# Optimization experiments

Hardware: AMD Instinct MI355X
Metric: run time of the kernel (lower is better)

The kernel has to match this reference:

```python
import jax, jax.numpy as jnp
import numpy as np

B = 16384
N_HIDDEN_TYPE = 16   # n_hidden option count (first block of output columns)
N_ACTIVE_TYPE = 8
N_OUT = N_HIDDEN_TYPE + N_ACTIVE_TYPE   # 24, also LSTM input size
H = 24                                   # LSTM hidden size (hardcoded in module)
LAYER_LIMIT = 24
STEPS = 2 * LAYER_LIMIT - 1              # 47


def setup_inputs() -> dict:
    key = jax.random.key(0)
    ks = jax.random.split(key, 7)
    s = 0.1
    return {
        "W_ih": jax.random.normal(ks[0], (4 * H, N_OUT), jnp.float32) * s,
        "W_hh": jax.random.normal(ks[1], (4 * H, H), jnp.float32) * s,
        "b_ih": jax.random.normal(ks[2], (4 * H,), jnp.float32) * s,
        "b_hh": jax.random.normal(ks[3], (4 * H,), jnp.float32) * s,
        "Wl": jax.random.normal(ks[4], (N_OUT, H), jnp.float32) * s,
        "bl": jax.random.normal(ks[5], (N_OUT,), jnp.float32) * s,
        "rand": jax.random.uniform(ks[6], (STEPS, B), jnp.float32),
    }


def reference(W_ih, W_hh, b_ih, b_hh, Wl, bl, rand):
    cols = jnp.arange(N_OUT)

    def step(carry, xs):
        h, c, a = carry
        i, r = xs  # i: step index (scalar), r: (B,) uniforms
        # PyTorch LSTMCell: gate order input, forget, cell, output
        gates = a @ W_ih.T + b_ih + h @ W_hh.T + b_hh
        ig, fg, gg, og = jnp.split(gates, 4, axis=1)
        c = jax.nn.sigmoid(fg) * c + jax.nn.sigmoid(ig) * jnp.tanh(gg)
        h = jax.nn.sigmoid(og) * jnp.tanh(c)
        logits = h @ Wl.T + bl  # (B, N_OUT)
        counter = (i + 1) // 2  # counter_nb_layers at an odd step
        mask = jnp.where(i % 2 == 1, cols < counter, cols >= N_HIDDEN_TYPE)
        p = jax.nn.softmax(jnp.where(mask, logits, -jnp.inf), axis=1)
        # stochastic sampling: first index where cumsum exceeds uniform
        act = jnp.argmax(jnp.cumsum(p, axis=1) > r[:, None], axis=1)
        pr = jnp.take_along_axis(p, act[:, None], axis=1)[:, 0]
        a_next = jax.nn.one_hot(act, N_OUT, dtype=logits.dtype)
        return (h, c, a_next), (pr, act)

    h0 = jnp.zeros((B, H), jnp.float32)
    c0 = jnp.zeros((B, H), jnp.float32)
    a0 = jnp.zeros((B, N_OUT), jnp.float32)
    _, (prob, actions) = jax.lax.scan(
        step, (h0, c0, a0), (jnp.arange(STEPS), rand))
    # stack over time -> (B, STEPS), actions as float like the numpy array
    return prob.T, actions.T.astype(jnp.float32)
```

## Files before the change

kernel.cpp:

```cpp
#include <hip/hip_runtime.h>
#include <math.h>

#define BATCH   16384
#define HD      24
#define NOUTC   24
#define NHID    16
#define NSTEPS  47
#define NG      96
#define GRP     32
#define NTG     12
#define JPW     2
#define GPW     8
#define THREADS 384

__device__ __forceinline__ float fast_sigmoid(float x) {
    float t = __expf(-x);
    return __builtin_amdgcn_rcpf(1.0f + t);
}
__device__ __forceinline__ float fast_tanh(float x) {
    float ax = fabsf(x);
    float t  = __expf(-2.0f * ax);
    float r  = (1.0f - t) * __builtin_amdgcn_rcpf(1.0f + t);
    return copysignf(r, x);
}

__global__ __launch_bounds__(THREADS) void policy_kernel(
    const float* __restrict__ W_ih, const float* __restrict__ W_hh,
    const float* __restrict__ b_ih, const float* __restrict__ b_hh,
    const float* __restrict__ Wl,   const float* __restrict__ bl,
    const float* __restrict__ rnd,  float* __restrict__ out)
{
    __shared__ float sWihB[NG][25];
    __shared__ float sBias[NG];
    __shared__ float sWhhP[HD][NTG][GPW];
    __shared__ float sWlP[HD][NTG][JPW];
    __shared__ float sBl[NOUTC];
    __shared__ float hh[HD][GRP];
    __shared__ float sL[NOUTC][GRP];
    __shared__ float sPr[GRP][NSTEPS + 2];
    __shared__ unsigned char sAct8[GRP][NSTEPS + 2];

    const int tid = threadIdx.x;
    const int w   = tid >> 5;
    const int e   = tid & 31;
    const int b   = blockIdx.x * GRP + e;

    for (int i = tid; i < NG * HD; i += THREADS) {
        int g = i / HD, k = i % HD;
        float bs = b_ih[g] + b_hh[g];
        sWihB[g][k] = W_ih[i] + bs;
        int t = g / 24, rem = g % 24;
        sWhhP[k][rem >> 1][t * JPW + (rem & 1)] = W_hh[i];
    }
    for (int i = tid; i < NOUTC * HD; i += THREADS) {
        int n = i / HD, k = i % HD;
        sWlP[k][n >> 1][n & 1] = Wl[i];
    }
    if (tid < NG)    sBias[tid] = b_ih[tid] + b_hh[tid];
    if (tid < NOUTC) sBl[tid]   = bl[tid];
    for (int i = tid; i < HD * GRP; i += THREADS) (&hh[0][0])[i] = 0.f;
    __syncthreads();

    float cst[JPW] = {0.f, 0.f};
    float accN[GPW];
    #pragma unroll
    for (int q = 0; q < GPW; ++q) accN[q] = 0.f;
    int act = 0;

    for (int s = 0; s < NSTEPS; ++s) {
        const float r = rnd[s * BATCH + b];

        float acc[GPW];
        if (s == 0) {
            #pragma unroll
            for (int t = 0; t < 4; ++t)
                #pragma unroll
                for (int i = 0; i < JPW; ++i)
                    acc[t * JPW + i] = accN[t * JPW + i] + sBias[t * 24 + w * JPW + i];
        } else {
            #pragma unroll
            for (int t = 0; t < 4; ++t)
                #pragma unroll
                for (int i = 0; i < JPW; ++i)
                    acc[t * JPW + i] = accN[t * JPW + i] + sWihB[t * 24 + w * JPW + i][act];
        }

        #pragma unroll
        for (int i = 0; i < JPW; ++i) {
            float ig = acc[i], fg = acc[JPW + i], gg = acc[2 * JPW + i], og = acc[3 * JPW + i];
            float si = fast_sigmoid(ig);
            float sf = fast_sigmoid(fg);
            float so = fast_sigmoid(og);
            float tg = fast_tanh(gg);
            float cj = sf * cst[i] + si * tg;
            cst[i] = cj;
            hh[w * JPW + i][e] = so * fast_tanh(cj);
        }
        __syncthreads();

        float l0 = 0.f, l1 = 0.f;
        #pragma unroll
        for (int q = 0; q < GPW; ++q) accN[q] = 0.f;
        #pragma unroll 6
        for (int k = 0; k < HD; ++k) {
            float hk = hh[k][e];
            const float* wp = &sWhhP[k][w][0];
            float4 w0 = *(const float4*)&wp[0];
            float4 w1 = *(const float4*)&wp[4];
            float2 lv = *(const float2*)&sWlP[k][w][0];
            accN[0] = fmaf(hk, w0.x, accN[0]);
            accN[1] = fmaf(hk, w0.y, accN[1]);
            accN[2] = fmaf(hk, w0.z, accN[2]);
            accN[3] = fmaf(hk, w0.w, accN[3]);
            accN[4] = fmaf(hk, w1.x, accN[4]);
            accN[5] = fmaf(hk, w1.y, accN[5]);
            accN[6] = fmaf(hk, w1.z, accN[6]);
            accN[7] = fmaf(hk, w1.w, accN[7]);
            l0 = fmaf(hk, lv.x, l0);
            l1 = fmaf(hk, lv.y, l1);
        }
        sL[w * JPW + 0][e] = l0 + sBl[w * JPW + 0];
        sL[w * JPW + 1][e] = l1 + sBl[w * JPW + 1];
        __syncthreads();

        const int  cnt = (s + 1) >> 1;
        const bool odd = (s & 1) != 0;
        float v[NOUTC];
        #pragma unroll
        for (int n = 0; n < NOUTC; ++n) v[n] = sL[n][e];
        float Z = 0.f, cum = 0.f, ea = 0.f, m = -INFINITY;
        int a = 0;
        bool found = false;
        if (odd) {
            #pragma unroll
            for (int n = 0; n < NOUTC; ++n) m = fmaxf(m, (n < cnt) ? v[n] : -INFINITY);
            #pragma unroll
            for (int n = 0; n < NOUTC; ++n) v[n] = (n < cnt) ? __expf(v[n] - m) : 0.f;
            #pragma unroll
            for (int n = 0; n < NOUTC; ++n) Z += v[n];
            const float rZ = r * Z;
            #pragma unroll
            for (int n = 0; n < NOUTC; ++n) {
                cum += v[n];
                if (!found && cum > rZ) { found = true; a = n; ea = v[n]; }
            }
            if (!found) { a = 0; ea = v[0]; }
        } else {
            #pragma unroll
            for (int n = NHID; n < NOUTC; ++n) m = fmaxf(m, v[n]);
            #pragma unroll
            for (int n = NHID; n < NOUTC; ++n) v[n] = __expf(v[n] - m);
            #pragma unroll
            for (int n = NHID; n < NOUTC; ++n) Z += v[n];
            const float rZ = r * Z;
            #pragma unroll
            for (int n = NHID; n < NOUTC; ++n) {
                cum += v[n];
                if (!found && cum > rZ) { found = true; a = n; ea = v[n]; }
            }
            if (!found) { a = 0; ea = 0.f; }
        }
        float pr = ea / Z;

        if (w == 0) { sPr[e][s] = pr; sAct8[e][s] = (unsigned char)a; }
        act = a;
    }

    __syncthreads();
    const int base = blockIdx.x * GRP * NSTEPS;
    for (int i = tid; i < GRP * NSTEPS; i += THREADS) {
        int rr = i / NSTEPS, ss = i - rr * NSTEPS;
        out[base + i]                          = sPr[rr][ss];
        out[(size_t)BATCH * NSTEPS + base + i] = (float)sAct8[rr][ss];
    }
}

extern "C" void kernel_launch(void* const* d_in, const int* in_sizes, int n_in,
                              void* d_out, int out_size, void* d_ws, size_t ws_size,
                              hipStream_t stream) {
    const float* W_ih = (const float*)d_in[0];
    const float* W_hh = (const float*)d_in[1];
    const float* b_ih = (const float*)d_in[2];
    const float* b_hh = (const float*)d_in[3];
    const float* Wl   = (const float*)d_in[4];
    const float* bl   = (const float*)d_in[5];
    const float* rnd  = (const float*)d_in[6];
    float* o = (float*)d_out;

    policy_kernel<<<BATCH / GRP, THREADS, 0, stream>>>(W_ih, W_hh, b_ih, b_hh, Wl, bl, rnd, o);
}
```

Measured before the change: 181.3 us.

## Keep each batch element within one wavefront and exchange hidden state via shuffles

The kernel is remapped so that each 64-lane wavefront holds 8 batch elements, with 8 gate-groups of 3 hidden units per element. Hidden state and logits now move between lanes with __shfl rather than through shared memory, which removes both __syncthreads from every one of the 47 steps. The block shrinks to 256 threads, each doing more FMAs (12 gate accumulators plus 3 logits). The cost is many cross-lane shuffles per step and higher register pressure from the fully unrolled loop.

```diff
diff --git a/kernel.cpp b/kernel.cpp
--- a/kernel.cpp
+++ b/kernel.cpp
@@ -7,11 +7,13 @@
 #define NHID    16
 #define NSTEPS  47
 #define NG      96
+#define NTG     8
+#define JPW     3
+#define GPW     12
+#define EPW     8
+#define WAVES   4
 #define GRP     32
-#define NTG     12
-#define JPW     2
-#define GPW     8
-#define THREADS 384
+#define THREADS 256
 
 __device__ __forceinline__ float fast_sigmoid(float x) {
     float t = __expf(-x);
@@ -32,106 +34,115 @@
 {
     __shared__ float sWihB[NG][25];
     __shared__ float sBias[NG];
-    __shared__ float sWhhP[HD][NTG][GPW];
-    __shared__ float sWlP[HD][NTG][JPW];
+    __shared__ __align__(16) float sWhhP[HD][NTG][GPW];
+    __shared__ __align__(16) float sWlP[HD][NTG][4];
     __shared__ float sBl[NOUTC];
-    __shared__ float hh[HD][GRP];
-    __shared__ float sL[NOUTC][GRP];
-    __shared__ float sPr[GRP][NSTEPS + 2];
-    __shared__ unsigned char sAct8[GRP][NSTEPS + 2];
-
-    const int tid = threadIdx.x;
-    const int w   = tid >> 5;
-    const int e   = tid & 31;
-    const int b   = blockIdx.x * GRP + e;
+    __shared__ float sPr[GRP][NSTEPS + 1];
+    __shared__ unsigned char sAct8[GRP][NSTEPS + 1];
+
+    const int tid  = threadIdx.x;
+    const int lane = tid & 63;
+    const int wv   = tid >> 6;
+    const int g    = lane >> 3;
+    const int e8   = lane & 7;
+    const int elem = wv * EPW + e8;
+    const int b    = blockIdx.x * GRP + elem;
 
     for (int i = tid; i < NG * HD; i += THREADS) {
-        int g = i / HD, k = i % HD;
-        float bs = b_ih[g] + b_hh[g];
-        sWihB[g][k] = W_ih[i] + bs;
-        int t = g / 24, rem = g % 24;
-        sWhhP[k][rem >> 1][t * JPW + (rem & 1)] = W_hh[i];
+        int gg = i / HD, k = i % HD;
+        float bs = b_ih[gg] + b_hh[gg];
+        sWihB[gg][k] = W_ih[i] + bs;
+        int t = gg / 24, rem = gg % 24;
+        sWhhP[k][rem / 3][t * 3 + rem % 3] = W_hh[i];
     }
     for (int i = tid; i < NOUTC * HD; i += THREADS) {
         int n = i / HD, k = i % HD;
-        sWlP[k][n >> 1][n & 1] = Wl[i];
+        sWlP[k][n / 3][n % 3] = Wl[i];
     }
     if (tid < NG)    sBias[tid] = b_ih[tid] + b_hh[tid];
     if (tid < NOUTC) sBl[tid]   = bl[tid];
-    for (int i = tid; i < HD * GRP; i += THREADS) (&hh[0][0])[i] = 0.f;
     __syncthreads();
 
-    float cst[JPW] = {0.f, 0.f};
+    float cst[JPW]  = {0.f, 0.f, 0.f};
+    float hloc[JPW] = {0.f, 0.f, 0.f};
     float accN[GPW];
     #pragma unroll
     for (int q = 0; q < GPW; ++q) accN[q] = 0.f;
-    int act = 0;
+    int actE = 0;
 
     for (int s = 0; s < NSTEPS; ++s) {
         const float r = rnd[s * BATCH + b];
 
-        float acc[GPW];
+        float a_[GPW];
         if (s == 0) {
             #pragma unroll
             for (int t = 0; t < 4; ++t)
                 #pragma unroll
                 for (int i = 0; i < JPW; ++i)
-                    acc[t * JPW + i] = accN[t * JPW + i] + sBias[t * 24 + w * JPW + i];
+                    a_[t * JPW + i] = accN[t * JPW + i] + sBias[t * 24 + 3 * g + i];
         } else {
             #pragma unroll
             for (int t = 0; t < 4; ++t)
                 #pragma unroll
                 for (int i = 0; i < JPW; ++i)
-                    acc[t * JPW + i] = accN[t * JPW + i] + sWihB[t * 24 + w * JPW + i][act];
+                    a_[t * JPW + i] = accN[t * JPW + i] + sWihB[t * 24 + 3 * g + i][actE];
         }
 
         #pragma unroll
         for (int i = 0; i < JPW; ++i) {
-            float ig = acc[i], fg = acc[JPW + i], gg = acc[2 * JPW + i], og = acc[3 * JPW + i];
+            float ig = a_[i], fg = a_[JPW + i], gg_ = a_[2 * JPW + i], og = a_[3 * JPW + i];
             float si = fast_sigmoid(ig);
             float sf = fast_sigmoid(fg);
             float so = fast_sigmoid(og);
-            float tg = fast_tanh(gg);
+            float tg = fast_tanh(gg_);
             float cj = sf * cst[i] + si * tg;
             cst[i] = cj;
-            hh[w * JPW + i][e] = so * fast_tanh(cj);
-        }
-        __syncthreads();
-
-        float l0 = 0.f, l1 = 0.f;
+            hloc[i] = so * fast_tanh(cj);
+        }
+
+        float l0 = 0.f, l1 = 0.f, l2 = 0.f;
         #pragma unroll
         for (int q = 0; q < GPW; ++q) accN[q] = 0.f;
-        #pragma unroll 6
+        #pragma unroll
         for (int k = 0; k < HD; ++k) {
-            float hk = hh[k][e];
-            const float* wp = &sWhhP[k][w][0];
-            float4 w0 = *(const float4*)&wp[0];
-            float4 w1 = *(const float4*)&wp[4];
-            float2 lv = *(const float2*)&sWlP[k][w][0];
-            accN[0] = fmaf(hk, w0.x, accN[0]);
-            accN[1] = fmaf(hk, w0.y, accN[1]);
-            accN[2] = fmaf(hk, w0.z, accN[2]);
-            accN[3] = fmaf(hk, w0.w, accN[3]);
-            accN[4] = fmaf(hk, w1.x, accN[4]);
-            accN[5] = fmaf(hk, w1.y, accN[5]);
-            accN[6] = fmaf(hk, w1.z, accN[6]);
-            accN[7] = fmaf(hk, w1.w, accN[7]);
+            float hown = (k % 3 == 0) ? hloc[0] : (k % 3 == 1) ? hloc[1] : hloc[2];
+            float hk = __shfl(hown, (k / 3) * NTG + e8, 64);
+            float4 w0 = *(const float4*)&sWhhP[k][g][0];
+            float4 w1 = *(const float4*)&sWhhP[k][g][4];
+            float4 w2 = *(const float4*)&sWhhP[k][g][8];
+            accN[0]  = fmaf(hk, w0.x, accN[0]);
+            accN[1]  = fmaf(hk, w0.y, accN[1]);
+            accN[2]  = fmaf(hk, w0.z, accN[2]);
+            accN[3]  = fmaf(hk, w0.w, accN[3]);
+            accN[4]  = fmaf(hk, w1.x, accN[4]);
+            accN[5]  = fmaf(hk, w1.y, accN[5]);
+            accN[6]  = fmaf(hk, w1.z, accN[6]);
+            accN[7]  = fmaf(hk, w1.w, accN[7]);
+            accN[8]  = fmaf(hk, w2.x, accN[8]);
+            accN[9]  = fmaf(hk, w2.y, accN[9]);
+            accN[10] = fmaf(hk, w2.z, accN[10]);
+            accN[11] = fmaf(hk, w2.w, accN[11]);
+            float4 lv = *(const float4*)&sWlP[k][g][0];
             l0 = fmaf(hk, lv.x, l0);
             l1 = fmaf(hk, lv.y, l1);
-        }
-        sL[w * JPW + 0][e] = l0 + sBl[w * JPW + 0];
-        sL[w * JPW + 1][e] = l1 + sBl[w * JPW + 1];
-        __syncthreads();
+            l2 = fmaf(hk, lv.z, l2);
+        }
+        l0 += sBl[3 * g + 0];
+        l1 += sBl[3 * g + 1];
+        l2 += sBl[3 * g + 2];
 
         const int  cnt = (s + 1) >> 1;
         const bool odd = (s & 1) != 0;
-        float v[NOUTC];
-        #pragma unroll
-        for (int n = 0; n < NOUTC; ++n) v[n] = sL[n][e];
-        float Z = 0.f, cum = 0.f, ea = 0.f, m = -INFINITY;
+        float Z = 0.f, cum = 0.f, ea = 0.f, m = -INFINITY, pr;
         int a = 0;
         bool found = false;
         if (odd) {
+            float v[NOUTC];
+            #pragma unroll
+            for (int n = 0; n < NOUTC; ++n) {
+                float sv = (n % 3 == 0) ? l0 : (n % 3 == 1) ? l1 : l2;
+                v[n] = __shfl(sv, (n / 3) * NTG + e8, 64);
+            }
             #pragma unroll
             for (int n = 0; n < NOUTC; ++n) m = fmaxf(m, (n < cnt) ? v[n] : -INFINITY);
             #pragma unroll
@@ -145,25 +156,33 @@
                 if (!found && cum > rZ) { found = true; a = n; ea = v[n]; }
             }
             if (!found) { a = 0; ea = v[0]; }
+            pr = ea / Z;
         } else {
-            #pragma unroll
-            for (int n = NHID; n < NOUTC; ++n) m = fmaxf(m, v[n]);
-            #pragma unroll
-            for (int n = NHID; n < NOUTC; ++n) v[n] = __expf(v[n] - m);
-            #pragma unroll
-            for (int n = NHID; n < NOUTC; ++n) Z += v[n];
+            float v8[8];
+            #pragma unroll
+            for (int i = 0; i < 8; ++i) {
+                int n = NHID + i;
+                float sv = (n % 3 == 0) ? l0 : (n % 3 == 1) ? l1 : l2;
+                v8[i] = __shfl(sv, (n / 3) * NTG + e8, 64);
+            }
+            #pragma unroll
+            for (int i = 0; i < 8; ++i) m = fmaxf(m, v8[i]);
+            #pragma unroll
+            for (int i = 0; i < 8; ++i) v8[i] = __expf(v8[i] - m);
+            #pragma unroll
+            for (int i = 0; i < 8; ++i) Z += v8[i];
             const float rZ = r * Z;
             #pragma unroll
-            for (int n = NHID; n < NOUTC; ++n) {
-                cum += v[n];
-                if (!found && cum > rZ) { found = true; a = n; ea = v[n]; }
+            for (int i = 0; i < 8; ++i) {
+                cum += v8[i];
+                if (!found && cum > rZ) { found = true; a = NHID + i; ea = v8[i]; }
             }
             if (!found) { a = 0; ea = 0.f; }
-        }
-        float pr = ea / Z;
-
-        if (w == 0) { sPr[e][s] = pr; sAct8[e][s] = (unsigned char)a; }
-        act = a;
+            pr = ea / Z;
+        }
+
+        if (g == 0) { sPr[elem][s] = pr; sAct8[elem][s] = (unsigned char)a; }
+        actE = a;
     }
 
     __syncthreads();
```

Measured after the change: 213.4 us. 17.8% more time.
